# Performance work log

Measured on AMD Instinct MI355X. Metric: run time of the kernel, lower is better.

The kernel has to match this reference:

```python
import jax, jax.numpy as jnp
import numpy as np

N_NODES = 100000
HIDDEN = 128


def _gcn_conv(x, edge_index, W, b, n_nodes):
    # PyG GCNConv with default symmetric normalization and self-loops.
    src, dst = edge_index[0], edge_index[1]
    loop = jnp.arange(n_nodes, dtype=src.dtype)
    src = jnp.concatenate([src, loop])
    dst = jnp.concatenate([dst, loop])
    # degree over destination nodes (edge weight = 1), self-loops included
    deg = jax.ops.segment_sum(jnp.ones_like(dst, dtype=x.dtype), dst,
                              num_segments=n_nodes)
    dinv = jax.lax.rsqrt(deg)  # deg >= 1 because of self-loops
    norm = dinv[src] * dinv[dst]  # [E+N]
    h = x @ W  # [N, 4H] linear transform first (d_in -> 4H)
    msg = norm[:, None] * h[src]  # [E+N, 4H]
    out = jax.ops.segment_sum(msg, dst, num_segments=n_nodes)
    return out + b


def setup_inputs() -> dict:
    key = jax.random.key(0)
    k1, k2, k3, k4, k5, k6 = jax.random.split(key, 6)
    n, h = N_NODES, HIDDEN
    x = jax.random.normal(k1, (n, h), dtype=jnp.float32)
    h_cur = jax.random.normal(k2, (n, h), dtype=jnp.float32)
    c_cur = jax.random.normal(k3, (n, h), dtype=jnp.float32)
    edge_index = jax.random.randint(k4, (2, 3200000), 0, n, dtype=jnp.int64)
    W = jax.random.normal(k5, (h, 4 * h), dtype=jnp.float32) / np.sqrt(h)
    b = jax.random.normal(k6, (4 * h,), dtype=jnp.float32) * 0.01
    return {"x": x, "edge_index": edge_index, "h_cur": h_cur,
            "c_cur": c_cur, "W": W, "b": b}


def reference(x, edge_index, h_cur, c_cur, W, b):
    combined = x + h_cur  # fused input + hidden add
    conv = _gcn_conv(combined, edge_index, W, b, x.shape[0])  # [N, 4H]
    cc_f = conv[:, :HIDDEN]  # first gate chunk (module returns cc_f only)
    return cc_f
```

## Files before the change

### kernel.cpp

```cpp
#include <hip/hip_runtime.h>
#include <hip/hip_bf16.h>

#define HID 128
#define BSH 6
#define MAXBUCK 2048

__device__ __forceinline__ float b2f(unsigned short u) {
    union { unsigned i; float f; } v; v.i = ((unsigned)u) << 16; return v.f;
}
__device__ __forceinline__ unsigned short f2b(float f) {
    unsigned u = __float_as_uint(f);
    return (unsigned short)((u + 0x7fffu + ((u >> 16) & 1u)) >> 16);
}

__global__ void zero_kernel(unsigned* __restrict__ p, int n) {
    int i = blockIdx.x * blockDim.x + threadIdx.x;
    if (i < n) p[i] = 0u;
}

__global__ __launch_bounds__(256) void bincount_kernel(const int* __restrict__ ei,
                                                       unsigned* __restrict__ bcount,
                                                       int E, int n, int nbuck) {
    __shared__ unsigned hist[MAXBUCK];
    for (int i = threadIdx.x; i < nbuck; i += 256) hist[i] = 0u;
    __syncthreads();
    int i = blockIdx.x * 256 + threadIdx.x, stride = gridDim.x * 256;
    for (; i < E; i += stride) {
        int dst = ei[(size_t)E + i];
        if ((unsigned)dst < (unsigned)n) atomicAdd(&hist[dst >> BSH], 1u);
    }
    __syncthreads();
    for (int b = threadIdx.x; b < nbuck; b += 256) {
        unsigned c = hist[b];
        if (c) atomicAdd(&bcount[b], c);
    }
}

__global__ __launch_bounds__(1024) void bscan_kernel(const unsigned* __restrict__ bcount,
                                                     unsigned* __restrict__ boff,
                                                     unsigned* __restrict__ bwoff,
                                                     unsigned* __restrict__ off,
                                                     int nbuck, int n) {
    __shared__ unsigned sums[1024];
    int t = threadIdx.x;
    int chunk = (nbuck + 1023) >> 10;
    int beg = min(t * chunk, nbuck), end = min(beg + chunk, nbuck);
    unsigned local = 0;
    for (int i = beg; i < end; ++i) local += bcount[i];
    sums[t] = local;
    __syncthreads();
    for (int d = 1; d < 1024; d <<= 1) {
        unsigned v = (t >= d) ? sums[t - d] : 0u;
        __syncthreads();
        sums[t] += v;
        __syncthreads();
    }
    unsigned run = (t > 0) ? sums[t - 1] : 0u;
    for (int i = beg; i < end; ++i) { boff[i] = run; bwoff[i] = run; run += bcount[i]; }
    if (t == 1023) { boff[nbuck] = sums[1023]; off[n] = sums[1023]; }
}

__global__ __launch_bounds__(256) void phase3_kernel(const int* __restrict__ ei,
                                                     unsigned* __restrict__ bwoff,
                                                     unsigned* __restrict__ binned,
                                                     const float* __restrict__ x,
                                                     const float* __restrict__ hc,
                                                     const float* __restrict__ W,
                                                     unsigned short* __restrict__ hp,
                                                     int E, int n, int nbuck, int nsb) {
    __shared__ union {
        struct { unsigned hist[MAXBUCK]; unsigned base[MAXBUCK]; } bs;
        float A[64 * 132];
    } sm;

    if (blockIdx.x < nsb) {
        int chunk = (E + nsb - 1) / nsb;
        int beg = blockIdx.x * chunk, end = min(E, beg + chunk);
        for (int i = threadIdx.x; i < nbuck; i += 256) sm.bs.hist[i] = 0u;
        __syncthreads();
        for (int i = beg + threadIdx.x; i < end; i += 256) {
            int dst = ei[(size_t)E + i];
            if ((unsigned)dst < (unsigned)n) atomicAdd(&sm.bs.hist[dst >> BSH], 1u);
        }
        __syncthreads();
        for (int b = threadIdx.x; b < nbuck; b += 256) {
            unsigned c = sm.bs.hist[b];
            sm.bs.base[b] = c ? atomicAdd(&bwoff[b], c) : 0u;
            sm.bs.hist[b] = 0u;
        }
        __syncthreads();
        for (int i = beg + threadIdx.x; i < end; i += 256) {
            int s = ei[i];
            int dst = ei[(size_t)E + i];
            if ((unsigned)dst >= (unsigned)n) continue;
            unsigned ss = (unsigned)min(max(s, 0), n - 1);
            int b = dst >> BSH;
            unsigned r = atomicAdd(&sm.bs.hist[b], 1u);
            binned[sm.bs.base[b] + r] = ss | ((unsigned)(dst & ((1 << BSH) - 1)) << 20);
        }
    } else {
        int tid = threadIdx.x;
        int r0 = (blockIdx.x - nsb) * 64;

        for (int i = tid; i < 2048; i += 256) {
            int row = i >> 5;
            int c4 = (i & 31) * 4;
            int grow = r0 + row;
            float4 v;
            if (grow < n) {
                float4 a = *(const float4*)(x + (size_t)grow * HID + c4);
                float4 bb = *(const float4*)(hc + (size_t)grow * HID + c4);
                v = make_float4(a.x + bb.x, a.y + bb.y, a.z + bb.z, a.w + bb.w);
            } else {
                v = make_float4(0.f, 0.f, 0.f, 0.f);
            }
            *(float4*)(&sm.A[row * 132 + c4]) = v;
        }
        __syncthreads();

        int cg = tid & 31;
        int c4 = cg * 4;
        int rg = tid >> 5;
        float acc[8][4];
#pragma unroll
        for (int r = 0; r < 8; ++r) {
            acc[r][0] = 0.f; acc[r][1] = 0.f; acc[r][2] = 0.f; acc[r][3] = 0.f;
        }

#pragma unroll 4
        for (int k = 0; k < 128; ++k) {
            float4 w = *(const float4*)(W + (size_t)k * 512 + c4);
#pragma unroll
            for (int r = 0; r < 8; ++r) {
                float a = sm.A[(rg * 8 + r) * 132 + k];
                acc[r][0] += a * w.x;
                acc[r][1] += a * w.y;
                acc[r][2] += a * w.z;
                acc[r][3] += a * w.w;
            }
        }

#pragma unroll
        for (int r = 0; r < 8; ++r) {
            int grow = r0 + rg * 8 + r;
            if (grow < n) {
                unsigned long long pack =
                    (unsigned long long)f2b(acc[r][0]) |
                    ((unsigned long long)f2b(acc[r][1]) << 16) |
                    ((unsigned long long)f2b(acc[r][2]) << 32) |
                    ((unsigned long long)f2b(acc[r][3]) << 48);
                *(unsigned long long*)(hp + (size_t)grow * HID + c4) = pack;
            }
        }
    }
}

__global__ __launch_bounds__(256) void csrbuild_kernel(const unsigned* __restrict__ binned,
                                                       const unsigned* __restrict__ boff,
                                                       unsigned* __restrict__ off,
                                                       float* __restrict__ dinv,
                                                       unsigned* __restrict__ srcs,
                                                       unsigned short* __restrict__ hp,
                                                       int n) {
    __shared__ unsigned hist[64];
    __shared__ unsigned nodeoff[64];
    __shared__ float sdinv[64];
    int b = blockIdx.x;
    unsigned s0 = boff[b], s1 = boff[b + 1];
    int t = threadIdx.x;
    if (t < 64) hist[t] = 0u;
    __syncthreads();
    for (unsigned j = s0 + t; j < s1; j += 256) atomicAdd(&hist[binned[j] >> 20], 1u);
    __syncthreads();
    if (t < 64) {
        unsigned cnt = hist[t];
        unsigned x = cnt;
        for (int d = 1; d < 64; d <<= 1) {
            unsigned v = __shfl_up(x, d, 64);
            if (t >= d) x += v;
        }
        unsigned excl = x - cnt;
        nodeoff[t] = excl;
        hist[t] = 0u;
        float dv = rsqrtf((float)(cnt + 1u));
        sdinv[t] = dv;
        int node = (b << BSH) + t;
        if (node < n) {
            off[node] = s0 + excl;
            dinv[node] = dv;
        }
    }
    __syncthreads();
    for (unsigned j = s0 + t; j < s1; j += 256) {
        unsigned p = binned[j];
        unsigned dl = p >> 20, s = p & 0xFFFFFu;
        unsigned r = atomicAdd(&hist[dl], 1u);
        srcs[s0 + nodeoff[dl] + r] = s;
    }
    int node0 = b << BSH;
    unsigned* hp32 = (unsigned*)hp;
    for (int idx = t; idx < 4096; idx += 256) {
        int nd = node0 + (idx >> 6);
        if (nd < n) {
            float dv = sdinv[idx >> 6];
            unsigned* p = hp32 + (size_t)nd * 64 + (idx & 63);
            unsigned u = *p;
            float lo = b2f((unsigned short)(u & 0xFFFFu)) * dv;
            float hi = b2f((unsigned short)(u >> 16)) * dv;
            *p = (unsigned)f2b(lo) | ((unsigned)f2b(hi) << 16);
        }
    }
}

__global__ __launch_bounds__(256) void agg_kernel(const unsigned* __restrict__ srcs,
                                                  const unsigned* __restrict__ off,
                                                  const float* __restrict__ dinv,
                                                  const unsigned short* __restrict__ hp,
                                                  const float* __restrict__ b,
                                                  float* __restrict__ out, int n) {
    int wid = (int)((blockIdx.x * (size_t)blockDim.x + threadIdx.x) >> 6);
    int lane = threadIdx.x & 63;
    if (wid >= n) return;
    unsigned beg = off[wid], end = off[wid + 1];
    int c = lane * 2;
    float ax = 0.f, ay = 0.f;

    unsigned i = beg;
    for (; i + 16 <= end; i += 16) {
        unsigned s[16]; ushort2 v[16];
#pragma unroll
        for (int k = 0; k < 16; ++k) s[k] = srcs[i + k];
#pragma unroll
        for (int k = 0; k < 16; ++k) v[k] = *(const ushort2*)(hp + (size_t)s[k] * HID + c);
#pragma unroll
        for (int k = 0; k < 16; ++k) { ax += b2f(v[k].x); ay += b2f(v[k].y); }
    }
    if (i < end) {
        unsigned last = end - 1;
        unsigned s[16]; ushort2 v[16]; float m[16];
#pragma unroll
        for (int k = 0; k < 16; ++k) {
            unsigned j = i + k;
            m[k] = (j < end) ? 1.f : 0.f;
            s[k] = srcs[j < end ? j : last];
        }
#pragma unroll
        for (int k = 0; k < 16; ++k) v[k] = *(const ushort2*)(hp + (size_t)s[k] * HID + c);
#pragma unroll
        for (int k = 0; k < 16; ++k) {
            ax = fmaf(m[k], b2f(v[k].x), ax);
            ay = fmaf(m[k], b2f(v[k].y), ay);
        }
    }

    ushort2 vd = *(const ushort2*)(hp + (size_t)wid * HID + c);
    ax += b2f(vd.x);
    ay += b2f(vd.y);

    float di = dinv[wid];
    float2 bb = *(const float2*)(b + c);
    float2 res = make_float2(di * ax + bb.x, di * ay + bb.y);
    *(float2*)(out + (size_t)wid * HID + c) = res;
}

extern "C" void kernel_launch(void* const* d_in, const int* in_sizes, int n_in,
                              void* d_out, int out_size, void* d_ws, size_t ws_size,
                              hipStream_t stream) {
    const float* x = (const float*)d_in[0];
    const int* ei = (const int*)d_in[1];
    const float* hc = (const float*)d_in[2];
    const float* W = (const float*)d_in[4];
    const float* b = (const float*)d_in[5];
    float* out = (float*)d_out;

    int n = in_sizes[0] / HID;
    int E = in_sizes[1] / 2;
    int nbuck = (n + 63) >> BSH;
    int nsb = 256;

    char* ws = (char*)d_ws;
    unsigned* bcount = (unsigned*)(ws);
    unsigned* boff   = (unsigned*)(ws + 8192);
    unsigned* bwoff  = (unsigned*)(ws + 16384);
    unsigned* off    = (unsigned*)(ws + 24576);
    float*    dinv   = (float*)   (ws + 424592);
    unsigned* srcs   = (unsigned*)(ws + 824592);
    unsigned short* hp = (unsigned short*)(ws + 13624592);

    unsigned* binned = (unsigned*)d_out;

    zero_kernel<<<(nbuck + 255) / 256, 256, 0, stream>>>(bcount, nbuck);
    bincount_kernel<<<512, 256, 0, stream>>>(ei, bcount, E, n, nbuck);
    bscan_kernel<<<1, 1024, 0, stream>>>(bcount, boff, bwoff, off, nbuck, n);

    int gemm_blocks = (n + 63) / 64;
    phase3_kernel<<<nsb + gemm_blocks, 256, 0, stream>>>(ei, bwoff, binned, x, hc, W, hp,
                                                         E, n, nbuck, nsb);
    csrbuild_kernel<<<nbuck, 256, 0, stream>>>(binned, boff, off, dinv, srcs, hp, n);

    int agg_blocks = (n + 3) / 4;
    agg_kernel<<<agg_blocks, 256, 0, stream>>>(srcs, off, dinv, hp, b, out, n);
}
```

Measured before the change: 285.6 us.

## Tile feature matrix into 16-column slabs and aggregate per tile

Stores the bf16 transformed features in eight column tiles of 16 values (32 bytes per node per tile) instead of row-major 256-byte rows. The GEMM, the dinv scaling pass and the aggregation all change to match. In aggregation each lane group of 8 handles one node within one tile, and consecutive blocks cover the 8 tiles of the same 32 nodes, so the gather working set per tile (about 3.2 MB) can sit in cache. The cost is 32-byte random gathers instead of 256-byte ones, and the CSR index and offset lists are read 8 times.

New measurement: 320.4 us. +12.2%, slower.

```diff
diff --git a/kernel.cpp b/kernel.cpp
--- a/kernel.cpp
+++ b/kernel.cpp
@@ -4,6 +4,7 @@
 #define HID 128
 #define BSH 6
 #define MAXBUCK 2048
+#define NTILE 8
 
 __device__ __forceinline__ float b2f(unsigned short u) {
     union { unsigned i; float f; } v; v.i = ((unsigned)u) << 16; return v.f;
@@ -140,6 +141,8 @@
             }
         }
 
+        size_t tile = (size_t)(c4 >> 4);
+        int cin = c4 & 15;
 #pragma unroll
         for (int r = 0; r < 8; ++r) {
             int grow = r0 + rg * 8 + r;
@@ -149,7 +152,7 @@
                     ((unsigned long long)f2b(acc[r][1]) << 16) |
                     ((unsigned long long)f2b(acc[r][2]) << 32) |
                     ((unsigned long long)f2b(acc[r][3]) << 48);
-                *(unsigned long long*)(hp + (size_t)grow * HID + c4) = pack;
+                *(unsigned long long*)(hp + tile * (size_t)n * 16 + (size_t)grow * 16 + cin) = pack;
             }
         }
     }
@@ -199,11 +202,16 @@
     }
     int node0 = b << BSH;
     unsigned* hp32 = (unsigned*)hp;
+    size_t tstride = (size_t)n * 8;
     for (int idx = t; idx < 4096; idx += 256) {
-        int nd = node0 + (idx >> 6);
+        int t8 = idx >> 9;
+        int rem = idx & 511;
+        int ndl = rem >> 3;
+        int wq = rem & 7;
+        int nd = node0 + ndl;
         if (nd < n) {
-            float dv = sdinv[idx >> 6];
-            unsigned* p = hp32 + (size_t)nd * 64 + (idx & 63);
+            float dv = sdinv[ndl];
+            unsigned* p = hp32 + (size_t)t8 * tstride + (size_t)nd * 8 + wq;
             unsigned u = *p;
             float lo = b2f((unsigned short)(u & 0xFFFFu)) * dv;
             float hi = b2f((unsigned short)(u >> 16)) * dv;
@@ -212,55 +220,70 @@
     }
 }
 
-__global__ __launch_bounds__(256) void agg_kernel(const unsigned* __restrict__ srcs,
-                                                  const unsigned* __restrict__ off,
-                                                  const float* __restrict__ dinv,
-                                                  const unsigned short* __restrict__ hp,
-                                                  const float* __restrict__ b,
-                                                  float* __restrict__ out, int n) {
-    int wid = (int)((blockIdx.x * (size_t)blockDim.x + threadIdx.x) >> 6);
-    int lane = threadIdx.x & 63;
-    if (wid >= n) return;
-    unsigned beg = off[wid], end = off[wid + 1];
-    int c = lane * 2;
+__global__ __launch_bounds__(256) void agg_tiled_kernel(const unsigned* __restrict__ srcs,
+                                                        const unsigned* __restrict__ off,
+                                                        const float* __restrict__ dinv,
+                                                        const unsigned short* __restrict__ hp,
+                                                        const float* __restrict__ b,
+                                                        float* __restrict__ out, int n) {
+    int blk = blockIdx.x;
+    int t = blk & 7;
+    int grp = blk >> 3;
+    int tid = threadIdx.x;
+    int w = tid >> 6;
+    int lane = tid & 63;
+    int ndw = lane >> 3;
+    int cp = lane & 7;
+    int node = grp * 32 + w * 8 + ndw;
+    bool valid = node < n;
+    int nd = valid ? node : (n - 1);
+    const unsigned short* hpt = hp + (size_t)t * n * 16;
+
+    unsigned base = off[nd];
+    unsigned cnt = valid ? (off[nd + 1] - base) : 0u;
+
     float ax = 0.f, ay = 0.f;
-
-    unsigned i = beg;
-    for (; i + 16 <= end; i += 16) {
-        unsigned s[16]; ushort2 v[16];
-#pragma unroll
-        for (int k = 0; k < 16; ++k) s[k] = srcs[i + k];
-#pragma unroll
-        for (int k = 0; k < 16; ++k) v[k] = *(const ushort2*)(hp + (size_t)s[k] * HID + c);
-#pragma unroll
-        for (int k = 0; k < 16; ++k) { ax += b2f(v[k].x); ay += b2f(v[k].y); }
-    }
-    if (i < end) {
-        unsigned last = end - 1;
-        unsigned s[16]; ushort2 v[16]; float m[16];
-#pragma unroll
-        for (int k = 0; k < 16; ++k) {
-            unsigned j = i + k;
-            m[k] = (j < end) ? 1.f : 0.f;
-            s[k] = srcs[j < end ? j : last];
-        }
-#pragma unroll
-        for (int k = 0; k < 16; ++k) v[k] = *(const ushort2*)(hp + (size_t)s[k] * HID + c);
-#pragma unroll
-        for (int k = 0; k < 16; ++k) {
-            ax = fmaf(m[k], b2f(v[k].x), ax);
-            ay = fmaf(m[k], b2f(v[k].y), ay);
-        }
-    }
-
-    ushort2 vd = *(const ushort2*)(hp + (size_t)wid * HID + c);
-    ax += b2f(vd.x);
-    ay += b2f(vd.y);
-
-    float di = dinv[wid];
-    float2 bb = *(const float2*)(b + c);
-    float2 res = make_float2(di * ax + bb.x, di * ay + bb.y);
-    *(float2*)(out + (size_t)wid * HID + c) = res;
+    unsigned k = 0;
+    for (; k + 8 <= cnt; k += 8) {
+        unsigned s[8]; unsigned v[8];
+#pragma unroll
+        for (int j = 0; j < 8; ++j) s[j] = srcs[base + k + j];
+#pragma unroll
+        for (int j = 0; j < 8; ++j) v[j] = *(const unsigned*)(hpt + (size_t)s[j] * 16 + cp * 2);
+#pragma unroll
+        for (int j = 0; j < 8; ++j) {
+            ax += b2f((unsigned short)(v[j] & 0xFFFFu));
+            ay += b2f((unsigned short)(v[j] >> 16));
+        }
+    }
+    if (k < cnt) {
+        unsigned last = cnt - 1;
+        unsigned s[8]; unsigned v[8]; float m[8];
+#pragma unroll
+        for (int j = 0; j < 8; ++j) {
+            unsigned jj = k + j;
+            m[j] = (jj < cnt) ? 1.f : 0.f;
+            s[j] = srcs[base + (jj < cnt ? jj : last)];
+        }
+#pragma unroll
+        for (int j = 0; j < 8; ++j) v[j] = *(const unsigned*)(hpt + (size_t)s[j] * 16 + cp * 2);
+#pragma unroll
+        for (int j = 0; j < 8; ++j) {
+            ax = fmaf(m[j], b2f((unsigned short)(v[j] & 0xFFFFu)), ax);
+            ay = fmaf(m[j], b2f((unsigned short)(v[j] >> 16)), ay);
+        }
+    }
+
+    if (valid) {
+        unsigned vd = *(const unsigned*)(hpt + (size_t)nd * 16 + cp * 2);
+        ax += b2f((unsigned short)(vd & 0xFFFFu));
+        ay += b2f((unsigned short)(vd >> 16));
+        float di = dinv[nd];
+        int col = t * 16 + cp * 2;
+        float2 bb = *(const float2*)(b + col);
+        float2 res = make_float2(di * ax + bb.x, di * ay + bb.y);
+        *(float2*)(out + (size_t)nd * HID + col) = res;
+    }
 }
 
 extern "C" void kernel_launch(void* const* d_in, const int* in_sizes, int n_in,
@@ -298,6 +321,6 @@
                                                          E, n, nbuck, nsb);
     csrbuild_kernel<<<nbuck, 256, 0, stream>>>(binned, boff, off, dinv, srcs, hp, n);
 
-    int agg_blocks = (n + 3) / 4;
-    agg_kernel<<<agg_blocks, 256, 0, stream>>>(srcs, off, dinv, hp, b, out, n);
-}
+    int ngrp = (n + 31) / 32;
+    agg_tiled_kernel<<<ngrp * NTILE, 256, 0, stream>>>(srcs, off, dinv, hp, b, out, n);
+}
```
